# Kernel tuning notes

Measured on AMD Instinct MI355X. Metric: run time of the kernel, lower is better.

## Reference

```python
import jax, jax.numpy as jnp
import numpy as np

B, S, HID, NH, HD, RD = 1, 2048, 2560, 32, 80, 64
SCALE = HD ** -0.5
NEG = -1e9


def _alibi_slopes(n):
    # n = 32 is a power of two -> standard geometric slopes 2^(-8i/n)
    return jnp.asarray(2.0 ** (-8.0 * np.arange(1, n + 1) / n), dtype=jnp.float32)


def _rope(x, pos):
    # GPT-NeoX style rotary on the first RD dims of each head; x: [B,S,NH,HD]
    inv_freq = 1.0 / (10000.0 ** (np.arange(0, RD, 2, dtype=np.float32) / RD))  # [RD/2]
    ang = pos.astype(jnp.float32)[..., None] * jnp.asarray(inv_freq)  # [B,S,RD/2]
    cos = jnp.cos(ang)[:, :, None, :]  # [B,S,1,RD/2]
    sin = jnp.sin(ang)[:, :, None, :]
    x1 = x[..., : RD // 2]
    x2 = x[..., RD // 2 : RD]
    rot = jnp.concatenate([x1 * cos - x2 * sin, x2 * cos + x1 * sin], axis=-1)
    return jnp.concatenate([rot, x[..., RD:]], axis=-1)


def setup_inputs() -> dict:
    key = jax.random.key(0)
    k1, k2, k3 = jax.random.split(key, 3)
    return {
        "position_ids": jnp.arange(B * S, dtype=jnp.int32).reshape(B, S) % S,
        "hidden_states": jax.random.normal(k1, (B, S, HID), dtype=jnp.float32),
        "w_qkv": jax.random.normal(k2, (HID, 3 * HID), dtype=jnp.float32) * 0.02,
        "w_out": jax.random.normal(k3, (HID, HID), dtype=jnp.float32) * 0.02,
    }


def reference(position_ids, hidden_states, w_qkv, w_out):
    qkv = hidden_states @ w_qkv                       # [B,S,3*HID]
    q, k, v = jnp.split(qkv, 3, axis=-1)
    q = _rope(q.reshape(B, S, NH, HD), position_ids)
    k = _rope(k.reshape(B, S, NH, HD), position_ids)
    v = v.reshape(B, S, NH, HD)

    scores = jnp.einsum("bqhd,bkhd->bhqk", q, k) * SCALE  # [B,NH,S,S]
    rel = (position_ids[:, None, :] - position_ids[:, :, None]).astype(jnp.float32)  # j - i
    slopes = _alibi_slopes(NH)
    bias = slopes[None, :, None, None] * rel[:, None, :, :]  # [B,NH,S,S]
    causal = rel <= 0.0
    scores = jnp.where(causal[:, None, :, :], scores + bias, NEG)
    attn = jax.nn.softmax(scores, axis=-1)
    out = jnp.einsum("bhqk,bkhd->bqhd", attn, v).reshape(B, S, HID)
    return out @ w_out
```

## Files before the change

### kernel.cpp

```cpp
#include <hip/hip_runtime.h>
#include <type_traits>
#include <utility>

typedef unsigned short u16;
typedef unsigned int u32;
typedef __attribute__((ext_vector_type(8))) short short8;
typedef __attribute__((ext_vector_type(8))) __bf16 bhalf8;
typedef __attribute__((ext_vector_type(4))) short short4v;
typedef __attribute__((ext_vector_type(4))) __bf16 bhalf4;
typedef __attribute__((ext_vector_type(4))) float f32x4;
typedef __attribute__((ext_vector_type(4))) unsigned short us4;

#define S_LEN 2048
#define NHEAD 32
#define HD 80
#define HDP 96
#define HID 2560
#define N3 7680
#define QK_SCALE 0.11180339887498949f
#define LOG2E 1.4426950408889634f

template <typename T, typename = void> struct MfmaTakes : std::false_type {};
template <typename T>
struct MfmaTakes<T, std::void_t<decltype(__builtin_amdgcn_mfma_f32_16x16x32_bf16(
                       std::declval<T>(), std::declval<T>(), std::declval<f32x4>(), 0, 0, 0))>>
    : std::true_type {};

template <typename AB>
__device__ inline f32x4 mfma_raw(AB a, AB b, f32x4 c) {
  return __builtin_amdgcn_mfma_f32_16x16x32_bf16(a, b, c, 0, 0, 0);
}
using mfma_ab_t = std::conditional_t<MfmaTakes<bhalf8>::value, bhalf8, short8>;
__device__ inline f32x4 MFMA(short8 a, short8 b, f32x4 c) {
  return mfma_raw<mfma_ab_t>(__builtin_bit_cast(mfma_ab_t, a),
                             __builtin_bit_cast(mfma_ab_t, b), c);
}

#if defined(__has_builtin)
#if __has_builtin(__builtin_amdgcn_mfma_f32_16x16x16bf16_1k)
#define MFMA16_RAW(a, b, c) __builtin_amdgcn_mfma_f32_16x16x16bf16_1k(a, b, c, 0, 0, 0)
#define HAVE_MFMA16 1
#elif __has_builtin(__builtin_amdgcn_mfma_f32_16x16x16_bf16)
#define MFMA16_RAW(a, b, c) __builtin_amdgcn_mfma_f32_16x16x16_bf16(a, b, c, 0, 0, 0)
#define HAVE_MFMA16 1
#endif
#endif

#ifdef HAVE_MFMA16
template <typename T, typename = void> struct M16Takes : std::false_type {};
template <typename T>
struct M16Takes<T, std::void_t<decltype(MFMA16_RAW(std::declval<T>(), std::declval<T>(),
                                                   std::declval<f32x4>()))>> : std::true_type {};
using m16_t = std::conditional_t<M16Takes<bhalf4>::value, bhalf4, short4v>;
__device__ inline f32x4 MFMA16(short4v a, short4v b, f32x4 c) {
  return MFMA16_RAW(__builtin_bit_cast(m16_t, a), __builtin_bit_cast(m16_t, b), c);
}
#else
__device__ inline f32x4 MFMA16(short4v a, short4v b, f32x4 c) {
  short8 a8 = {a[0], a[1], a[2], a[3], 0, 0, 0, 0};
  short8 b8 = {b[0], b[1], b[2], b[3], 0, 0, 0, 0};
  return MFMA(a8, b8, c);
}
#endif

__device__ inline float bf2f(u16 b) { return __uint_as_float(((u32)b) << 16); }
__device__ inline u16 f2bf(float f) {
  u32 u = __float_as_uint(f);
  u += 0x7fffu + ((u >> 16) & 1u);
  return (u16)(u >> 16);
}

typedef __attribute__((address_space(1))) void as1_void;
typedef __attribute__((address_space(3))) void as3_void;

#if defined(__has_builtin)
#if __has_builtin(__builtin_amdgcn_global_load_lds)
#define HAVE_GLL 1
#endif
#endif

__device__ inline void stage16(const u16* g, u16* lds_base, int lane) {
#ifdef HAVE_GLL
  (void)lane;
  __builtin_amdgcn_global_load_lds((as1_void*)g, (as3_void*)lds_base, 16, 0, 0);
#else
  *(short8*)(lds_base + lane * 8) = *(const short8*)g;
#endif
}

__device__ inline void sched_barrier0() {
#if defined(__has_builtin)
#if __has_builtin(__builtin_amdgcn_sched_barrier)
  __builtin_amdgcn_sched_barrier(0);
#endif
#endif
}

__global__ __launch_bounds__(256) void detect_dtype(const u32* __restrict__ words,
                                                    int* __restrict__ flag) {
  __shared__ int red[256];
  int junk = 0;
  for (int i = threadIdx.x; i < 2048; i += 256) {
    u16 lo = (u16)(words[i] & 0xffffu);
    u32 e = (lo >> 7) & 0xffu;
    junk += (e >= 137u);
  }
  red[threadIdx.x] = junk;
  __syncthreads();
  for (int s = 128; s > 0; s >>= 1) {
    if (threadIdx.x < s) red[threadIdx.x] += red[threadIdx.x + s];
    __syncthreads();
  }
  if (threadIdx.x == 0) flag[0] = (red[0] > 64) ? 1 : 0;
}

__global__ __launch_bounds__(256) void convert_hidden(const void* __restrict__ in,
                                                      u16* __restrict__ out, int n4,
                                                      const int* __restrict__ flagp) {
  const int f = *flagp;
  int i = blockIdx.x * 256 + threadIdx.x;
  if (i >= n4) return;
  if (f) {
    const float* inf = (const float*)in;
    us4 o;
#pragma unroll
    for (int j = 0; j < 4; ++j) o[j] = f2bf(inf[(size_t)i * 4 + j]);
    *(us4*)&out[(size_t)i * 4] = o;
  } else {
    *(us4*)&out[(size_t)i * 4] = *(const us4*)&((const u16*)in)[(size_t)i * 4];
  }
}

__global__ __launch_bounds__(256) void transpose64(const void* __restrict__ in,
                                                   u16* __restrict__ out,
                                                   int istride, int ioff, int ostride,
                                                   const int* __restrict__ flagp) {
  __shared__ u16 tile[64][66];
  const int f = flagp ? *flagp : 0;
  const int bx = blockIdx.x * 64, by = blockIdx.y * 64;
  const int tx4 = (threadIdx.x & 15) * 4, ty = threadIdx.x >> 4;
#pragma unroll
  for (int i = 0; i < 4; ++i) {
    const int row = ty + i * 16;
    const size_t idx = (size_t)(by + row) * istride + ioff + bx + tx4;
    us4 v;
    if (f) {
      const f32x4 x = *(const f32x4*)&((const float*)in)[idx];
#pragma unroll
      for (int j = 0; j < 4; ++j) v[j] = f2bf(x[j]);
    } else {
      v = *(const us4*)&((const u16*)in)[idx];
    }
    *(u32*)&tile[row][tx4] = (u32)v[0] | ((u32)v[1] << 16);
    *(u32*)&tile[row][tx4 + 2] = (u32)v[2] | ((u32)v[3] << 16);
  }
  __syncthreads();
#pragma unroll
  for (int i = 0; i < 4; ++i) {
    const int oc = ty + i * 16;
    us4 o;
#pragma unroll
    for (int j = 0; j < 4; ++j) o[j] = tile[tx4 + j][oc];
    *(us4*)&out[(size_t)(bx + oc) * ostride + by + tx4] = o;
  }
}

__global__ __launch_bounds__(256, 2) void gemm128c(const u16* __restrict__ A,
                                                   const u16* __restrict__ Bt,
                                                   void* __restrict__ C,
                                                   int M, int N, int K,
                                                   const int* __restrict__ flagp) {
  __shared__ u16 As[2][128 * 64];
  __shared__ u16 Bs[3][128 * 64];
  const int tid = threadIdx.x;
  const int w = tid >> 6, l = tid & 63, la = l & 15, qd = l >> 4;
  const int wr = w >> 1, wc = w & 1;
  const int of32 = flagp ? *flagp : 0;

  const int nbx = gridDim.x;
  const int nwg = nbx * gridDim.y;
  int lin = blockIdx.y * nbx + blockIdx.x;
  if ((nwg & 7) == 0) lin = (lin & 7) * (nwg >> 3) + (lin >> 3);
  const int m0 = (lin / nbx) * 128, n0 = (lin % nbx) * 128;
  const int NT = K >> 6;

  const int sx0 = (qd ^ (la & 7)) * 8;
  const int sx1 = ((4 + qd) ^ (la & 7)) * 8;
  const int gsw = ((tid & 7) ^ ((tid >> 3) & 7)) * 8;

  f32x4 acc[4][4] = {};

  auto issue = [&](int s) {
    if (s >= NT * 4) return;
    const int kt = s >> 2, part = s & 3;
    const int h = part & 1;
    const u16* G = (part >= 2) ? A : Bt;
    const int b0 = (part >= 2) ? m0 : n0;
    u16* L = ((part >= 2) ? &As[kt & 1][0] : &Bs[kt % 3][0]) + h * 4096;
    const int k0 = kt << 6;
#pragma unroll
    for (int q = 0; q < 2; ++q) {
      const int row = h * 64 + q * 32 + (tid >> 3);
      const u16* g = G + (size_t)(b0 + row) * K + k0 + gsw;
      stage16(g, L + (q * 256 + w * 64) * 8, l);
    }
  };

  auto readA = [&](int buf, int mh, short8(&af)[2][2]) {
    const u16* base = &As[buf][0];
#pragma unroll
    for (int i = 0; i < 2; ++i) {
      const int ro = (wr * 64 + mh * 32 + i * 16 + la) * 64;
      af[i][0] = *(const short8*)(base + ro + sx0);
      af[i][1] = *(const short8*)(base + ro + sx1);
    }
  };
  auto readB = [&](int buf, int nh, short8(&bf)[2][2]) {
    const u16* base = &Bs[buf][0];
#pragma unroll
    for (int j = 0; j < 2; ++j) {
      const int ro = (wc * 64 + nh * 32 + j * 16 + la) * 64;
      bf[j][0] = *(const short8*)(base + ro + sx0);
      bf[j][1] = *(const short8*)(base + ro + sx1);
    }
  };
  auto quad = [&](short8(&af)[2][2], short8(&bf)[2][2], int mh, int nh) {
#pragma unroll
    for (int kk = 0; kk < 2; ++kk)
#pragma unroll
      for (int i = 0; i < 2; ++i)
#pragma unroll
        for (int jj = 0; jj < 2; ++jj)
          acc[mh * 2 + i][nh * 2 + jj] =
              MFMA(af[i][kk], bf[jj][kk], acc[mh * 2 + i][nh * 2 + jj]);
  };

#pragma unroll
  for (int s = 0; s < 6; ++s) issue(s);
  asm volatile("s_waitcnt vmcnt(4)" ::: "memory");
  __builtin_amdgcn_s_barrier();

  for (int t = 0; t < NT; ++t) {
    const int ab = t & 1, bb = t % 3;
    short8 af[2][2], af2[2][2], bf0[2][2], bf1[2][2];
    readA(ab, 0, af);
    sched_barrier0();
    readB(bb, 0, bf0);
    sched_barrier0();
    readB(bb, 1, bf1);
    sched_barrier0();
    issue(4 * t + 6);
    issue(4 * t + 7);
    issue(4 * t + 8);
    issue(4 * t + 9);
    asm volatile("s_waitcnt lgkmcnt(4)" ::: "memory");
    sched_barrier0();
    readA(ab, 1, af2);
    sched_barrier0();
    __builtin_amdgcn_s_setprio(1);
    quad(af, bf0, 0, 0);
    __builtin_amdgcn_s_setprio(0);
    asm volatile("s_waitcnt lgkmcnt(4)" ::: "memory");
    sched_barrier0();
    __builtin_amdgcn_s_setprio(1);
    quad(af, bf1, 0, 1);
    __builtin_amdgcn_s_setprio(0);
    asm volatile("s_waitcnt lgkmcnt(0)" ::: "memory");
    sched_barrier0();
    __builtin_amdgcn_s_setprio(1);
    quad(af2, bf0, 1, 0);
    quad(af2, bf1, 1, 1);
    __builtin_amdgcn_s_setprio(0);
    asm volatile("s_waitcnt vmcnt(4)" ::: "memory");
    __builtin_amdgcn_s_barrier();
  }

#pragma unroll
  for (int i = 0; i < 4; ++i)
#pragma unroll
    for (int j = 0; j < 4; ++j) {
      const int r0 = m0 + wr * 64 + (i >> 1) * 32 + (i & 1) * 16 + qd * 4;
      const int c0 = n0 + wc * 64 + (j >> 1) * 32 + (j & 1) * 16 + la;
#pragma unroll
      for (int r = 0; r < 4; ++r) {
        if (of32)
          ((float*)C)[(size_t)(r0 + r) * N + c0] = acc[i][j][r];
        else
          ((u16*)C)[(size_t)(r0 + r) * N + c0] = f2bf(acc[i][j][r]);
      }
    }
}

__global__ __launch_bounds__(512, 2) void gemm256(const u16* __restrict__ A,
                                                  const u16* __restrict__ Bt,
                                                  u16* __restrict__ C,
                                                  int M, int N, int K) {
  __shared__ u16 As[2][256 * 64];
  __shared__ u16 Bs[3][256 * 64];
  const int tid = threadIdx.x;
  const int w = tid >> 6, l = tid & 63, la = l & 15, qd = l >> 4;
  const int wr = w >> 2, wc = w & 3;

  const int nbx = gridDim.x;
  const int nwg = nbx * gridDim.y;
  int lin = blockIdx.y * nbx + blockIdx.x;
  if ((nwg & 7) == 0) lin = (lin & 7) * (nwg >> 3) + (lin >> 3);
  const int m0 = (lin / nbx) * 256, n0 = (lin % nbx) * 256;
  const int NT = K >> 6;

  const int sx0 = (qd ^ (la & 7)) * 8;
  const int sx1 = ((4 + qd) ^ (la & 7)) * 8;
  const int gsw = ((tid & 7) ^ ((tid >> 3) & 7)) * 8;

  f32x4 acc[8][4] = {};

  auto issue = [&](int s) {
    if (s >= NT * 4) return;
    const int kt = s >> 2, part = s & 3;
    const int h = part & 1;
    const u16* G = (part >= 2) ? A : Bt;
    const int b0 = (part >= 2) ? m0 : n0;
    u16* L = ((part >= 2) ? &As[kt & 1][0] : &Bs[kt % 3][0]) + h * 8192;
    const int k0 = kt << 6;
#pragma unroll
    for (int q = 0; q < 2; ++q) {
      const int row = h * 128 + q * 64 + (tid >> 3);
      const u16* g = G + (size_t)(b0 + row) * K + k0 + gsw;
      stage16(g, L + (q * 512 + w * 64) * 8, l);
    }
  };

  auto readA = [&](int buf, int mh, short8(&af)[4][2]) {
    const u16* base = &As[buf][0];
#pragma unroll
    for (int i = 0; i < 4; ++i) {
      const int ro = (wr * 128 + mh * 64 + i * 16 + la) * 64;
      af[i][0] = *(const short8*)(base + ro + sx0);
      af[i][1] = *(const short8*)(base + ro + sx1);
    }
  };
  auto readB = [&](int buf, int nh, short8(&bf)[2][2]) {
    const u16* base = &Bs[buf][0];
#pragma unroll
    for (int j = 0; j < 2; ++j) {
      const int ro = (wc * 64 + nh * 32 + j * 16 + la) * 64;
      bf[j][0] = *(const short8*)(base + ro + sx0);
      bf[j][1] = *(const short8*)(base + ro + sx1);
    }
  };
  auto quad = [&](short8(&af)[4][2], short8(&bf)[2][2], int mh, int nh) {
#pragma unroll
    for (int kk = 0; kk < 2; ++kk)
#pragma unroll
      for (int i = 0; i < 4; ++i)
#pragma unroll
        for (int jj = 0; jj < 2; ++jj)
          acc[mh * 4 + i][nh * 2 + jj] =
              MFMA(af[i][kk], bf[jj][kk], acc[mh * 4 + i][nh * 2 + jj]);
  };

#pragma unroll
  for (int s = 0; s < 6; ++s) issue(s);
  asm volatile("s_waitcnt vmcnt(4)" ::: "memory");
  __builtin_amdgcn_s_barrier();

  for (int t = 0; t < NT; ++t) {
    const int ab = t & 1, bb = t % 3;
    short8 af[4][2], af2[4][2], bf0[2][2], bf1[2][2];
    readA(ab, 0, af);
    sched_barrier0();
    readB(bb, 0, bf0);
    sched_barrier0();
    readB(bb, 1, bf1);
    sched_barrier0();
    issue(4 * t + 6);
    issue(4 * t + 7);
    issue(4 * t + 8);
    issue(4 * t + 9);
    asm volatile("s_waitcnt lgkmcnt(4)" ::: "memory");
    sched_barrier0();
    readA(ab, 1, af2);
    sched_barrier0();
    __builtin_amdgcn_s_setprio(1);
    quad(af, bf0, 0, 0);
    __builtin_amdgcn_s_setprio(0);
    asm volatile("s_waitcnt lgkmcnt(8)" ::: "memory");
    sched_barrier0();
    __builtin_amdgcn_s_setprio(1);
    quad(af, bf1, 0, 1);
    __builtin_amdgcn_s_setprio(0);
    asm volatile("s_waitcnt lgkmcnt(0)" ::: "memory");
    sched_barrier0();
    __builtin_amdgcn_s_setprio(1);
    quad(af2, bf0, 1, 0);
    quad(af2, bf1, 1, 1);
    __builtin_amdgcn_s_setprio(0);
    asm volatile("s_waitcnt vmcnt(4)" ::: "memory");
    __builtin_amdgcn_s_barrier();
  }

#pragma unroll
  for (int i = 0; i < 8; ++i)
#pragma unroll
    for (int j = 0; j < 4; ++j) {
      const int r0 = m0 + wr * 128 + i * 16 + qd * 4;
      const int c0 = n0 + wc * 64 + j * 16 + la;
#pragma unroll
      for (int r = 0; r < 4; ++r)
        C[(size_t)(r0 + r) * N + c0] = f2bf(acc[i][j][r]);
    }
}

__global__ __launch_bounds__(256) void rope_prep(const u16* __restrict__ qkv,
                                                 const int* __restrict__ pos,
                                                 u16* __restrict__ Qh,
                                                 u16* __restrict__ Kt) {
  const int s = blockIdx.x;
  const int h = blockIdx.y * 4 + (threadIdx.x >> 6);
  const int t = threadIdx.x & 63;
  const size_t qin = (size_t)s * N3 + h * HD;
  const size_t kin = qin + HID;
  const size_t ob = ((size_t)h * S_LEN + s) * HDP;
  const size_t kb = ((size_t)(h * 32) + (s >> 6)) * 6144 + (size_t)(s & 63) * 8;
  if (t < 32) {
    const float p = (float)pos[s];
    const float inv = exp2f(-(float)t * (13.287712379549449f / 32.0f));
    const float ang = p * inv;
    const float cs = cosf(ang), sn = sinf(ang);
    float x1 = bf2f(qkv[qin + t]), x2 = bf2f(qkv[qin + t + 32]);
    Qh[ob + t] = f2bf(x1 * cs - x2 * sn);
    Qh[ob + t + 32] = f2bf(x2 * cs + x1 * sn);
    x1 = bf2f(qkv[kin + t]);
    x2 = bf2f(qkv[kin + t + 32]);
    Kt[kb + (size_t)(t >> 3) * 512 + (t & 7)] = f2bf(x1 * cs - x2 * sn);
    const int d2 = t + 32;
    Kt[kb + (size_t)(d2 >> 3) * 512 + (d2 & 7)] = f2bf(x2 * cs + x1 * sn);
  } else if (t < 48) {
    const int d = t + 32;
    Qh[ob + d] = qkv[qin + d];
    Kt[kb + (size_t)(d >> 3) * 512 + (d & 7)] = qkv[kin + d];
  } else {
    const int d = t + 32;
    Qh[ob + d] = 0;
    Kt[kb + (size_t)(d >> 3) * 512 + (d & 7)] = 0;
  }
}

__global__ __launch_bounds__(512, 4) void attn_fused(const u16* __restrict__ Qh,
                                                     const u16* __restrict__ Kt,
                                                     const u16* __restrict__ Vt,
                                                     u16* __restrict__ AO) {
  __shared__ u16 Ks[2][768 * 8];
  __shared__ u16 Vs[2][640 * 8];
  const int tid = threadIdx.x, w = tid >> 6, l = tid & 63;
  const int la = l & 15, qd = l >> 4;
  const int h = blockIdx.y;
  const int p = blockIdx.x;
  const int tile = (h < 16) ? p : 15 - p;
  const int q0 = tile * 128;
  const int nIt = 2 * tile + 2;
  const size_t hS = (size_t)h * S_LEN;

  const int qb = q0 + w * 16;
  const int q = qb + la;
  short8 qf[3];
#pragma unroll
  for (int c = 0; c < 3; ++c)
    qf[c] = *(const short8*)&Qh[(hS + qb + la) * HDP + c * 32 + qd * 8];

  const float slope2 = exp2f(-0.25f * (float)(h + 1)) * LOG2E;
  const float scl2 = QK_SCALE * LOG2E;
  float m_i = -1e30f, l_i = 0.f;
  f32x4 acc[5] = {};

  const u16* gK = Kt + (size_t)h * 32 * 6144;
  const u16* gV = Vt + (size_t)h * HD * S_LEN;

  auto stage = [&](int kt_g, int buf) {
    const u16* gkt = gK + (size_t)kt_g * 6144;
    stage16(gkt + (size_t)(w * 64 + l) * 8, &Ks[buf][(w * 64) * 8], l);
    if (w < 4)
      stage16(gkt + (size_t)(512 + w * 64 + l) * 8, &Ks[buf][(512 + w * 64) * 8], l);
    const u16* gv = gV + (kt_g << 6);
    {
      const int c = w * 64 + l;
      const int row = c >> 3, seg = c & 7;
      const int gcol = ((seg - (row & 7)) & 7) * 8;
      stage16(gv + (size_t)row * S_LEN + gcol, &Vs[buf][(w * 64) * 8], l);
    }
    if (w < 2) {
      const int c = 512 + w * 64 + l;
      const int row = c >> 3, seg = c & 7;
      const int gcol = ((seg - (row & 7)) & 7) * 8;
      stage16(gv + (size_t)row * S_LEN + gcol, &Vs[buf][(512 + w * 64) * 8], l);
    }
  };

  stage(0, 0);
  for (int it = 0; it < nIt; ++it) {
    const int buf = it & 1;
    __syncthreads();
    if (it + 1 < nIt) stage(it + 1, buf ^ 1);
    const int k0 = it << 6;
    if (k0 >= qb + 16) continue;

    f32x4 st[4];
#pragma unroll
    for (int kt = 0; kt < 4; ++kt) {
      short8 kf[3];
#pragma unroll
      for (int c = 0; c < 3; ++c)
        kf[c] = *(const short8*)&Ks[buf][((c * 4 + qd) * 64 + kt * 16 + la) * 8];
      f32x4 z = {};
#pragma unroll
      for (int c = 0; c < 3; ++c) z = MFMA(kf[c], qf[c], z);
      st[kt] = z;
    }

    const float base = (float)(k0 + qd * 4 - q);
    float mloc = -1e30f;
    if (k0 + 64 <= qb + 1) {
#pragma unroll
      for (int kt = 0; kt < 4; ++kt)
#pragma unroll
        for (int r = 0; r < 4; ++r) {
          const float rel = base + (float)(kt * 16 + r);
          const float v = st[kt][r] * scl2 + slope2 * rel;
          st[kt][r] = v;
          mloc = fmaxf(mloc, v);
        }
    } else {
#pragma unroll
      for (int kt = 0; kt < 4; ++kt)
#pragma unroll
        for (int r = 0; r < 4; ++r) {
          const float rel = base + (float)(kt * 16 + r);
          const float v = (rel <= 0.f) ? st[kt][r] * scl2 + slope2 * rel : -1e30f;
          st[kt][r] = v;
          mloc = fmaxf(mloc, v);
        }
    }
    mloc = fmaxf(mloc, __shfl_xor(mloc, 16));
    mloc = fmaxf(mloc, __shfl_xor(mloc, 32));

    if (!__all(mloc - m_i <= 8.0f)) {
      const float nm = fmaxf(m_i, mloc);
      const float al = exp2f(m_i - nm);
      m_i = nm;
      l_i *= al;
#pragma unroll
      for (int dt = 0; dt < 5; ++dt) acc[dt] *= al;
    }

    float ps = 0.f;
    short4v pf[4];
#pragma unroll
    for (int kt = 0; kt < 4; ++kt) {
      short4v pk;
#pragma unroll
      for (int r = 0; r < 4; ++r) {
        const float pv = exp2f(st[kt][r] - m_i);
        ps += pv;
        pk[r] = (short)f2bf(pv);
      }
      pf[kt] = pk;
    }
    ps += __shfl_xor(ps, 16);
    ps += __shfl_xor(ps, 32);
    l_i += ps;

    const int cb = qd * 4 + ((la & 7) << 3);
#pragma unroll
    for (int dt = 0; dt < 5; ++dt) {
      const int vrow = (dt * 16 + la) * 64;
#pragma unroll
      for (int kt = 0; kt < 4; ++kt) {
        const short4v vf = *(const short4v*)&Vs[buf][vrow + ((kt * 16 + cb) & 63)];
        acc[dt] = MFMA16(vf, pf[kt], acc[dt]);
      }
    }
  }

  const float inv = 1.0f / l_i;
  const size_t row = (size_t)q;
#pragma unroll
  for (int dt = 0; dt < 5; ++dt) {
    us4 o;
#pragma unroll
    for (int r = 0; r < 4; ++r) o[r] = f2bf(acc[dt][r] * inv);
    *(us4*)&AO[row * HID + h * HD + dt * 16 + qd * 4] = o;
  }
}

extern "C" void kernel_launch(void* const* d_in, const int* in_sizes, int n_in,
                              void* d_out, int out_size, void* d_ws, size_t ws_size,
                              hipStream_t stream) {
  const int* pos = (const int*)d_in[0];
  const void* hidden = d_in[1];
  const void* w_qkv = d_in[2];
  const void* w_out = d_in[3];
  u16* ws = (u16*)d_ws;

  u16* Hb = ws;
  u16* WtQ = Hb + (size_t)S_LEN * HID;
  u16* WtO = WtQ + (size_t)N3 * HID;
  u16* qkv = WtO + (size_t)HID * HID;
  int* flag = (int*)(qkv + (size_t)S_LEN * N3);
  u16* Vt = Hb;
  u16* Qh = WtQ;
  u16* Kh = Qh + (size_t)NHEAD * S_LEN * HDP;
  u16* AO = Kh + (size_t)NHEAD * S_LEN * HDP;

  detect_dtype<<<1, 256, 0, stream>>>((const u32*)hidden, flag);
  convert_hidden<<<(S_LEN * HID / 4 + 255) / 256, 256, 0, stream>>>(hidden, Hb,
                                                                    S_LEN * HID / 4, flag);
  transpose64<<<dim3(N3 / 64, HID / 64), 256, 0, stream>>>(w_qkv, WtQ, N3, 0, HID, flag);
  transpose64<<<dim3(HID / 64, HID / 64), 256, 0, stream>>>(w_out, WtO, HID, 0, HID, flag);
  gemm256<<<dim3(N3 / 256, S_LEN / 256), 512, 0, stream>>>(Hb, WtQ, qkv, S_LEN, N3, HID);
  transpose64<<<dim3(HID / 64, S_LEN / 64), 256, 0, stream>>>(qkv, Vt, N3, 2 * HID, S_LEN,
                                                              nullptr);
  rope_prep<<<dim3(S_LEN, NHEAD / 4), 256, 0, stream>>>(qkv, pos, Qh, Kh);
  attn_fused<<<dim3(16, NHEAD), 512, 0, stream>>>(Qh, Kh, Vt, AO);
  gemm128c<<<dim3(HID / 128, S_LEN / 128), 256, 0, stream>>>(AO, WtO, d_out, S_LEN, HID,
                                                             HID, flag);
}
```

Baseline: 372.8 us.

## Pair causal query tiles per attention block and merge weight transposes into one launch

```diff
diff --git a/kernel.cpp b/kernel.cpp
--- a/kernel.cpp
+++ b/kernel.cpp
@@ -162,6 +162,50 @@
 #pragma unroll
     for (int j = 0; j < 4; ++j) o[j] = tile[tx4 + j][oc];
     *(us4*)&out[(size_t)(bx + oc) * ostride + by + tx4] = o;
+  }
+}
+
+__global__ __launch_bounds__(256) void transpose_w2(const void* __restrict__ wq,
+                                                    u16* __restrict__ WtQ,
+                                                    const void* __restrict__ wo,
+                                                    u16* __restrict__ WtO,
+                                                    const int* __restrict__ flagp) {
+  __shared__ u16 tile[64][66];
+  const int f = *flagp;
+  const int bxr = blockIdx.x;
+  const void* in;
+  u16* out;
+  int istride, bx;
+  if (bxr < N3 / 64) {
+    in = wq; out = WtQ; istride = N3; bx = bxr * 64;
+  } else {
+    in = wo; out = WtO; istride = HID; bx = (bxr - N3 / 64) * 64;
+  }
+  const int by = blockIdx.y * 64;
+  const int tx4 = (threadIdx.x & 15) * 4, ty = threadIdx.x >> 4;
+#pragma unroll
+  for (int i = 0; i < 4; ++i) {
+    const int row = ty + i * 16;
+    const size_t idx = (size_t)(by + row) * istride + bx + tx4;
+    us4 v;
+    if (f) {
+      const f32x4 x = *(const f32x4*)&((const float*)in)[idx];
+#pragma unroll
+      for (int j = 0; j < 4; ++j) v[j] = f2bf(x[j]);
+    } else {
+      v = *(const us4*)&((const u16*)in)[idx];
+    }
+    *(u32*)&tile[row][tx4] = (u32)v[0] | ((u32)v[1] << 16);
+    *(u32*)&tile[row][tx4 + 2] = (u32)v[2] | ((u32)v[3] << 16);
+  }
+  __syncthreads();
+#pragma unroll
+  for (int i = 0; i < 4; ++i) {
+    const int oc = ty + i * 16;
+    us4 o;
+#pragma unroll
+    for (int j = 0; j < 4; ++j) o[j] = tile[tx4 + j][oc];
+    *(us4*)&out[(size_t)(bx + oc) * HID + by + tx4] = o;
   }
 }
 
@@ -446,27 +490,30 @@
   }
 }
 
-__global__ __launch_bounds__(512, 4) void attn_fused(const u16* __restrict__ Qh,
-                                                     const u16* __restrict__ Kt,
-                                                     const u16* __restrict__ Vt,
-                                                     u16* __restrict__ AO) {
+__global__ __launch_bounds__(256) void attn_fused(const u16* __restrict__ Qh,
+                                                  const u16* __restrict__ Kt,
+                                                  const u16* __restrict__ Vt,
+                                                  u16* __restrict__ AO) {
   __shared__ u16 Ks[2][768 * 8];
   __shared__ u16 Vs[2][640 * 8];
   const int tid = threadIdx.x, w = tid >> 6, l = tid & 63;
   const int la = l & 15, qd = l >> 4;
   const int h = blockIdx.y;
-  const int p = blockIdx.x;
-  const int tile = (h < 16) ? p : 15 - p;
-  const int q0 = tile * 128;
-  const int nIt = 2 * tile + 2;
+  const int x = blockIdx.x;
+  const int pair = x >> 1;
+  const int half = (x & 1) ^ (h >> 4);
+  const int q0A = (15 - pair) * 128 + half * 64;
+  const int q0B = pair * 128 + half * 64;
+  const int nItA = (q0A >> 6) + 1;
+  const int nItB = (q0B >> 6) + 1;
   const size_t hS = (size_t)h * S_LEN;
 
-  const int qb = q0 + w * 16;
-  const int q = qb + la;
-  short8 qf[3];
-#pragma unroll
-  for (int c = 0; c < 3; ++c)
-    qf[c] = *(const short8*)&Qh[(hS + qb + la) * HDP + c * 32 + qd * 8];
+  short8 qfA[3], qfB[3];
+#pragma unroll
+  for (int c = 0; c < 3; ++c) {
+    qfA[c] = *(const short8*)&Qh[(hS + q0A + w * 16 + la) * HDP + c * 32 + qd * 8];
+    qfB[c] = *(const short8*)&Qh[(hS + q0B + w * 16 + la) * HDP + c * 32 + qd * 8];
+  }
 
   const float slope2 = exp2f(-0.25f * (float)(h + 1)) * LOG2E;
   const float scl2 = QK_SCALE * LOG2E;
@@ -478,118 +525,129 @@
 
   auto stage = [&](int kt_g, int buf) {
     const u16* gkt = gK + (size_t)kt_g * 6144;
-    stage16(gkt + (size_t)(w * 64 + l) * 8, &Ks[buf][(w * 64) * 8], l);
-    if (w < 4)
-      stage16(gkt + (size_t)(512 + w * 64 + l) * 8, &Ks[buf][(512 + w * 64) * 8], l);
+#pragma unroll
+    for (int j = 0; j < 3; ++j)
+      stage16(gkt + (size_t)(j * 256 + tid) * 8, &Ks[buf][(j * 256 + w * 64) * 8], l);
     const u16* gv = gV + (kt_g << 6);
-    {
-      const int c = w * 64 + l;
-      const int row = c >> 3, seg = c & 7;
-      const int gcol = ((seg - (row & 7)) & 7) * 8;
-      stage16(gv + (size_t)row * S_LEN + gcol, &Vs[buf][(w * 64) * 8], l);
-    }
-    if (w < 2) {
-      const int c = 512 + w * 64 + l;
-      const int row = c >> 3, seg = c & 7;
-      const int gcol = ((seg - (row & 7)) & 7) * 8;
-      stage16(gv + (size_t)row * S_LEN + gcol, &Vs[buf][(512 + w * 64) * 8], l);
-    }
-  };
-
+#pragma unroll
+    for (int j = 0; j < 3; ++j) {
+      const int c0 = j * 256 + w * 64;
+      if (c0 < 640) {
+        const int c = c0 + l;
+        const int row = c >> 3, seg = c & 7;
+        const int gcol = ((seg - (row & 7)) & 7) * 8;
+        stage16(gv + (size_t)row * S_LEN + gcol, &Vs[buf][c0 * 8], l);
+      }
+    }
+  };
+
+  int g = 0;
   stage(0, 0);
-  for (int it = 0; it < nIt; ++it) {
-    const int buf = it & 1;
-    __syncthreads();
-    if (it + 1 < nIt) stage(it + 1, buf ^ 1);
-    const int k0 = it << 6;
-    if (k0 >= qb + 16) continue;
-
-    f32x4 st[4];
-#pragma unroll
-    for (int kt = 0; kt < 4; ++kt) {
-      short8 kf[3];
-#pragma unroll
-      for (int c = 0; c < 3; ++c)
-        kf[c] = *(const short8*)&Ks[buf][((c * 4 + qd) * 64 + kt * 16 + la) * 8];
-      f32x4 z = {};
-#pragma unroll
-      for (int c = 0; c < 3; ++c) z = MFMA(kf[c], qf[c], z);
-      st[kt] = z;
-    }
-
-    const float base = (float)(k0 + qd * 4 - q);
-    float mloc = -1e30f;
-    if (k0 + 64 <= qb + 1) {
-#pragma unroll
-      for (int kt = 0; kt < 4; ++kt)
+
+  auto run_seg = [&](const short8(&qf)[3], int q0, int nIt, bool more) {
+    const int qb = q0 + w * 16;
+    const int q = qb + la;
+    for (int it = 0; it < nIt; ++it, ++g) {
+      const int buf = g & 1;
+      __syncthreads();
+      if (it + 1 < nIt) stage(it + 1, buf ^ 1);
+      else if (more) stage(0, buf ^ 1);
+      const int k0 = it << 6;
+      if (k0 >= qb + 16) continue;
+
+      f32x4 st[4];
+#pragma unroll
+      for (int kt = 0; kt < 4; ++kt) {
+        short8 kf[3];
+#pragma unroll
+        for (int c = 0; c < 3; ++c)
+          kf[c] = *(const short8*)&Ks[buf][((c * 4 + qd) * 64 + kt * 16 + la) * 8];
+        f32x4 z = {};
+#pragma unroll
+        for (int c = 0; c < 3; ++c) z = MFMA(kf[c], qf[c], z);
+        st[kt] = z;
+      }
+
+      const float base = (float)(k0 + qd * 4 - q);
+      float mloc = -1e30f;
+      if (k0 + 64 <= qb + 1) {
+#pragma unroll
+        for (int kt = 0; kt < 4; ++kt)
+#pragma unroll
+          for (int r = 0; r < 4; ++r) {
+            const float rel = base + (float)(kt * 16 + r);
+            const float v = st[kt][r] * scl2 + slope2 * rel;
+            st[kt][r] = v;
+            mloc = fmaxf(mloc, v);
+          }
+      } else {
+#pragma unroll
+        for (int kt = 0; kt < 4; ++kt)
+#pragma unroll
+          for (int r = 0; r < 4; ++r) {
+            const float rel = base + (float)(kt * 16 + r);
+            const float v = (rel <= 0.f) ? st[kt][r] * scl2 + slope2 * rel : -1e30f;
+            st[kt][r] = v;
+            mloc = fmaxf(mloc, v);
+          }
+      }
+      mloc = fmaxf(mloc, __shfl_xor(mloc, 16));
+      mloc = fmaxf(mloc, __shfl_xor(mloc, 32));
+
+      if (!__all(mloc - m_i <= 8.0f)) {
+        const float nm = fmaxf(m_i, mloc);
+        const float al = exp2f(m_i - nm);
+        m_i = nm;
+        l_i *= al;
+#pragma unroll
+        for (int dt = 0; dt < 5; ++dt) acc[dt] *= al;
+      }
+
+      float ps = 0.f;
+      short4v pf[4];
+#pragma unroll
+      for (int kt = 0; kt < 4; ++kt) {
+        short4v pk;
 #pragma unroll
         for (int r = 0; r < 4; ++r) {
-          const float rel = base + (float)(kt * 16 + r);
-          const float v = st[kt][r] * scl2 + slope2 * rel;
-          st[kt][r] = v;
-          mloc = fmaxf(mloc, v);
+          const float pv = exp2f(st[kt][r] - m_i);
+          ps += pv;
+          pk[r] = (short)f2bf(pv);
         }
-    } else {
-#pragma unroll
-      for (int kt = 0; kt < 4; ++kt)
-#pragma unroll
-        for (int r = 0; r < 4; ++r) {
-          const float rel = base + (float)(kt * 16 + r);
-          const float v = (rel <= 0.f) ? st[kt][r] * scl2 + slope2 * rel : -1e30f;
-          st[kt][r] = v;
-          mloc = fmaxf(mloc, v);
+        pf[kt] = pk;
+      }
+      ps += __shfl_xor(ps, 16);
+      ps += __shfl_xor(ps, 32);
+      l_i += ps;
+
+      const int cb = qd * 4 + ((la & 7) << 3);
+#pragma unroll
+      for (int dt = 0; dt < 5; ++dt) {
+        const int vrow = (dt * 16 + la) * 64;
+#pragma unroll
+        for (int kt = 0; kt < 4; ++kt) {
+          const short4v vf = *(const short4v*)&Vs[buf][vrow + ((kt * 16 + cb) & 63)];
+          acc[dt] = MFMA16(vf, pf[kt], acc[dt]);
         }
-    }
-    mloc = fmaxf(mloc, __shfl_xor(mloc, 16));
-    mloc = fmaxf(mloc, __shfl_xor(mloc, 32));
-
-    if (!__all(mloc - m_i <= 8.0f)) {
-      const float nm = fmaxf(m_i, mloc);
-      const float al = exp2f(m_i - nm);
-      m_i = nm;
-      l_i *= al;
-#pragma unroll
-      for (int dt = 0; dt < 5; ++dt) acc[dt] *= al;
-    }
-
-    float ps = 0.f;
-    short4v pf[4];
-#pragma unroll
-    for (int kt = 0; kt < 4; ++kt) {
-      short4v pk;
-#pragma unroll
-      for (int r = 0; r < 4; ++r) {
-        const float pv = exp2f(st[kt][r] - m_i);
-        ps += pv;
-        pk[r] = (short)f2bf(pv);
       }
-      pf[kt] = pk;
-    }
-    ps += __shfl_xor(ps, 16);
-    ps += __shfl_xor(ps, 32);
-    l_i += ps;
-
-    const int cb = qd * 4 + ((la & 7) << 3);
+    }
+    const float inv = 1.0f / l_i;
+    const size_t row = (size_t)q;
 #pragma unroll
     for (int dt = 0; dt < 5; ++dt) {
-      const int vrow = (dt * 16 + la) * 64;
-#pragma unroll
-      for (int kt = 0; kt < 4; ++kt) {
-        const short4v vf = *(const short4v*)&Vs[buf][vrow + ((kt * 16 + cb) & 63)];
-        acc[dt] = MFMA16(vf, pf[kt], acc[dt]);
-      }
-    }
-  }
-
-  const float inv = 1.0f / l_i;
-  const size_t row = (size_t)q;
-#pragma unroll
-  for (int dt = 0; dt < 5; ++dt) {
-    us4 o;
-#pragma unroll
-    for (int r = 0; r < 4; ++r) o[r] = f2bf(acc[dt][r] * inv);
-    *(us4*)&AO[row * HID + h * HD + dt * 16 + qd * 4] = o;
-  }
+      us4 o;
+#pragma unroll
+      for (int r = 0; r < 4; ++r) o[r] = f2bf(acc[dt][r] * inv);
+      *(us4*)&AO[row * HID + h * HD + dt * 16 + qd * 4] = o;
+    }
+    m_i = -1e30f;
+    l_i = 0.f;
+#pragma unroll
+    for (int dt = 0; dt < 5; ++dt) acc[dt] = f32x4{};
+  };
+
+  run_seg(qfA, q0A, nItA, true);
+  run_seg(qfB, q0B, nItB, false);
 }
 
 extern "C" void kernel_launch(void* const* d_in, const int* in_sizes, int n_in,
@@ -614,13 +672,13 @@
   detect_dtype<<<1, 256, 0, stream>>>((const u32*)hidden, flag);
   convert_hidden<<<(S_LEN * HID / 4 + 255) / 256, 256, 0, stream>>>(hidden, Hb,
                                                                     S_LEN * HID / 4, flag);
-  transpose64<<<dim3(N3 / 64, HID / 64), 256, 0, stream>>>(w_qkv, WtQ, N3, 0, HID, flag);
-  transpose64<<<dim3(HID / 64, HID / 64), 256, 0, stream>>>(w_out, WtO, HID, 0, HID, flag);
+  transpose_w2<<<dim3(N3 / 64 + HID / 64, HID / 64), 256, 0, stream>>>(w_qkv, WtQ, w_out,
+                                                                       WtO, flag);
   gemm256<<<dim3(N3 / 256, S_LEN / 256), 512, 0, stream>>>(Hb, WtQ, qkv, S_LEN, N3, HID);
   transpose64<<<dim3(HID / 64, S_LEN / 64), 256, 0, stream>>>(qkv, Vt, N3, 2 * HID, S_LEN,
                                                               nullptr);
   rope_prep<<<dim3(S_LEN, NHEAD / 4), 256, 0, stream>>>(qkv, pos, Qh, Kh);
-  attn_fused<<<dim3(16, NHEAD), 512, 0, stream>>>(Qh, Kh, Vt, AO);
+  attn_fused<<<dim3(16, NHEAD), 256, 0, stream>>>(Qh, Kh, Vt, AO);
   gemm128c<<<dim3(HID / 128, S_LEN / 128), 256, 0, stream>>>(AO, WtO, d_out, S_LEN, HID,
                                                              HID, flag);
 }
```

Result: no change. 377.1 us (+1.2%).
